# Kernel tuning notes

Hardware: AMD Instinct MI355X
Metric: run time of the kernel (lower is better)

Reference implementation:

```python
import jax, jax.numpy as jnp
import numpy as np

B, NP, NS, CIN, COUT, CMID = 16, 1024, 32, 64, 128, 32

def _bn(x, g, b, m, v, eps=1e-5):
    # inference-mode BatchNorm over channel axis 1
    sh = (1, -1) + (1,) * (x.ndim - 2)
    return (x - m.reshape(sh)) * (g.reshape(sh) * jax.lax.rsqrt(v.reshape(sh) + eps)) + b.reshape(sh)

def setup_inputs() -> dict:
    key = jax.random.key(0)
    ks = jax.random.split(key, 10)
    f = jax.random.normal
    return {
        "new_xyz": f(ks[0], (B, 3, NP), jnp.float32),
        "grouped_xyz": f(ks[1], (B, NP, NS, 3), jnp.float32),
        "grouped_feature": f(ks[2], (B, CIN, NS, NP), jnp.float32),
        "wh_w": f(ks[3], (CMID, 3), jnp.float32) * 0.1,
        "wh_b": f(ks[4], (CMID,), jnp.float32) * 0.1,
        "wh_g": jnp.ones((CMID,), jnp.float32), "wh_beta": jnp.zeros((CMID,), jnp.float32),
        "wh_m": jnp.zeros((CMID,), jnp.float32), "wh_v": jnp.ones((CMID,), jnp.float32),
        "n1_w": f(ks[5], (16, 1), jnp.float32) * 0.1,
        "n1_b": f(ks[6], (16,), jnp.float32) * 0.1,
        "n1_g": jnp.ones((16,), jnp.float32), "n1_beta": jnp.zeros((16,), jnp.float32),
        "n1_m": jnp.zeros((16,), jnp.float32), "n1_v": jnp.ones((16,), jnp.float32),
        "n2_w": f(ks[7], (1, 16), jnp.float32) * 0.1,
        "n2_b": f(ks[8], (1,), jnp.float32) * 0.1,
        "n2_g": jnp.ones((1,), jnp.float32), "n2_beta": jnp.zeros((1,), jnp.float32),
        "n2_m": jnp.zeros((1,), jnp.float32), "n2_v": jnp.ones((1,), jnp.float32),
        "out_w": f(ks[9], (COUT, CIN, CMID), jnp.float32) * 0.05,
        "out_b": jnp.zeros((COUT,), jnp.float32),
        "out_g": jnp.ones((COUT,), jnp.float32), "out_beta": jnp.zeros((COUT,), jnp.float32),
        "out_m": jnp.zeros((COUT,), jnp.float32), "out_v": jnp.ones((COUT,), jnp.float32),
    }

def reference(new_xyz, grouped_xyz, grouped_feature,
              wh_w, wh_b, wh_g, wh_beta, wh_m, wh_v,
              n1_w, n1_b, n1_g, n1_beta, n1_m, n1_v,
              n2_w, n2_b, n2_g, n2_beta, n2_m, n2_v,
              out_w, out_b, out_g, out_beta, out_m, out_v):
    # kernel_density_estimation_ball mutates in place: after i=0 the reference
    # point is zero, so ONLY sample 0 is actually zeroed. Replicate exactly.
    gx = grouped_xyz.at[:, :, 0, :].set(0.0)          # [B,NP,NS,3]
    density = jnp.sum(gx, axis=-1, keepdims=True)      # [B,NP,NS,1]
    density = jnp.where(density < 1e-10, 1e-10, density)
    inv = 1.0 / density
    ds = inv / jnp.max(inv, axis=2, keepdims=True)     # [B,NP,NS,1]
    # weight net on the mutated grouped_xyz
    gx_p = jnp.transpose(gx, (0, 3, 1, 2))             # [B,3,NP,NS]
    w = jax.nn.relu(_bn(jnp.einsum('bcps,oc->bops', gx_p, wh_w) + wh_b.reshape(1, -1, 1, 1),
                        wh_g, wh_beta, wh_m, wh_v))    # [B,CMID,NP,NS]
    # nonlinear density transform
    dsp = jnp.transpose(ds, (0, 3, 1, 2))              # [B,1,NP,NS]
    d1 = jax.nn.relu(_bn(jnp.einsum('bcps,oc->bops', dsp, n1_w) + n1_b.reshape(1, -1, 1, 1),
                         n1_g, n1_beta, n1_m, n1_v))   # [B,16,NP,NS]
    d2 = jax.nn.sigmoid(_bn(jnp.einsum('bcps,oc->bops', d1, n2_w) + n2_b.reshape(1, -1, 1, 1),
                            n2_g, n2_beta, n2_m, n2_v))  # [B,1,NP,NS]
    # density-scaled features, then batched matmul with positional weights
    gf = jnp.transpose(grouped_feature, (0, 1, 3, 2)) * d2      # [B,CIN,NP,NS]
    mm = jnp.einsum('bcps,bmps->bcpm', gf, w)                   # [B,CIN,NP,CMID]
    # out_conv: Conv2d(CIN->COUT, kernel (1,CMID)) collapses last dim
    out = jnp.einsum('bcpk,ock->bop', mm, out_w) + out_b.reshape(1, -1, 1)  # [B,COUT,NP]
    out = _bn(out, out_g, out_beta, out_m, out_v)
    return (jnp.transpose(new_xyz, (0, 2, 1)), out)
```

## Files before the change

### kernel.cpp

```cpp
#include <hip/hip_runtime.h>
#include <hip/hip_bf16.h>


#define NPP 1024
#define NSS 32

typedef __attribute__((ext_vector_type(8))) short short8;
typedef __attribute__((ext_vector_type(4))) float f32x4;

__device__ __forceinline__ unsigned short f2bf(float x) {
  union { float f; unsigned u; } v; v.f = x;
  unsigned r = v.u + 0x7FFFu + ((v.u >> 16) & 1u);
  return (unsigned short)(r >> 16);
}

__device__ __forceinline__ unsigned long long pack4bf(f32x4 v) {
  return (unsigned long long)f2bf(v[0])
       | ((unsigned long long)f2bf(v[1]) << 16)
       | ((unsigned long long)f2bf(v[2]) << 32)
       | ((unsigned long long)f2bf(v[3]) << 48);
}

__global__ __launch_bounds__(256) void k_prep(
    const float* __restrict__ out_w, const float* __restrict__ new_xyz,
    unsigned short* __restrict__ owc, float* __restrict__ out0)
{
  int bid = blockIdx.x, t = threadIdx.x;
  if (bid < 128) {
    int gid = bid * 256 + t;
    int lane = gid & 63, ci = gid >> 6;
    int hi = ci & 1, tt = (ci >> 1) & 15, cblk = (ci >> 5) & 3, w = ci >> 7;
    int sg = lane >> 4, l15 = lane & 15;
    int o = w*32 + hi*16 + l15;
    int k = tt*2 + (sg >> 1);
    int cbase = cblk*16 + (sg & 1)*8;
    short8 vv;
    #pragma unroll
    for (int j = 0; j < 8; ++j)
      vv[j] = (short)f2bf(out_w[(o*64 + cbase + j)*32 + k]);
    *(short8*)&owc[(size_t)gid * 8] = vv;
  } else {
    int idx = (bid - 128) * 256 + t;
    int b = idx / 3072, r = idx - b*3072, p = r / 3, d = r - p*3;
    out0[idx] = new_xyz[(b*3 + d)*NPP + p];
  }
}

__global__ __launch_bounds__(256) void k_xpose(
    const float* __restrict__ F, unsigned short* __restrict__ Fb)
{
  int bid = blockIdx.x;
  int xcd = bid & 7, idx = bid >> 3;
  int b = xcd * 2 + (idx >> 4), ptq = idx & 15;
  int t = threadIdx.x;
  int sg = t >> 6, l15 = (t >> 2) & 15, k4 = t & 3;

  #pragma unroll
  for (int cblk = 0; cblk < 4; ++cblk) {
    int c = cblk * 16 + l15;
    const float* src = &F[((size_t)((b*64 + c)*32) + sg*8)*NPP + ptq*64 + k4*4];
    #pragma unroll
    for (int ptl = 0; ptl < 4; ++ptl) {
      float4 v[8];
      #pragma unroll
      for (int j = 0; j < 8; ++j) v[j] = *(const float4*)&src[(size_t)j*NPP + ptl*16];
      unsigned short* tb = &Fb[(size_t)(b*64 + ptq*4 + ptl)*32768 + cblk*512 + sg*128 + l15*8];
      #pragma unroll
      for (int pwl = 0; pwl < 4; ++pwl) {
        unsigned o0 = (unsigned)f2bf(((const float*)&v[0])[pwl]) | ((unsigned)f2bf(((const float*)&v[1])[pwl]) << 16);
        unsigned o1 = (unsigned)f2bf(((const float*)&v[2])[pwl]) | ((unsigned)f2bf(((const float*)&v[3])[pwl]) << 16);
        unsigned o2 = (unsigned)f2bf(((const float*)&v[4])[pwl]) | ((unsigned)f2bf(((const float*)&v[5])[pwl]) << 16);
        unsigned o3 = (unsigned)f2bf(((const float*)&v[6])[pwl]) | ((unsigned)f2bf(((const float*)&v[7])[pwl]) << 16);
        uint4 wv = {o0, o1, o2, o3};
        *(uint4*)&tb[(size_t)(k4*4 + pwl)*2048] = wv;
      }
    }
  }
}

struct Smem {
  union {
    unsigned short wd[16*32*32];
    char mm[2][16*1040];
  } u;
  float cst[192];
};

__global__ __launch_bounds__(256, 4) void k_main(
    const unsigned short* __restrict__ Fb, const float* __restrict__ GX,
    const float* __restrict__ whw, const float* __restrict__ whb,
    const float* __restrict__ whg, const float* __restrict__ whbeta,
    const float* __restrict__ whm, const float* __restrict__ whv,
    const float* __restrict__ n1w, const float* __restrict__ n1b,
    const float* __restrict__ n1g, const float* __restrict__ n1beta,
    const float* __restrict__ n1m, const float* __restrict__ n1v,
    const float* __restrict__ n2w, const float* __restrict__ n2b,
    const float* __restrict__ n2g, const float* __restrict__ n2beta,
    const float* __restrict__ n2m, const float* __restrict__ n2v,
    const unsigned short* __restrict__ OWc,
    const float* __restrict__ ob, const float* __restrict__ og,
    const float* __restrict__ obeta, const float* __restrict__ om,
    const float* __restrict__ ov,
    float* __restrict__ out1)
{
  __shared__ Smem sm;
  int bid = (blockIdx.x & 7) * 128 + (blockIdx.x >> 3);
  int b = bid >> 6, p0 = (bid & 63) << 4;
  int t = threadIdx.x, lane = t & 63, w = t >> 6;
  int l15 = lane & 15, sg = lane >> 4;
  int pl0 = w * 4;

  const unsigned short* ftile = &Fb[(size_t)(b*64 + (bid & 63))*32768 + sg*128 + l15*8];
  short8 af[4][4];
  #pragma unroll
  for (int cblk = 0; cblk < 4; ++cblk)
    #pragma unroll
    for (int i = 0; i < 4; ++i)
      af[cblk][i] = *(const short8*)&ftile[(size_t)(pl0 + i)*2048 + cblk*512];

  int pp = t >> 4, si = t & 15;
  float gxl[2][3]; float invv[2];
  #pragma unroll
  for (int u = 0; u < 2; ++u) {
    int s = si*2 + u;
    float x = 0.f, y = 0.f, z = 0.f;
    if (s != 0) {
      const float* g = &GX[(size_t)((b*NPP + p0 + pp)*NSS + s)*3];
      x = g[0]; y = g[1]; z = g[2];
    }
    gxl[u][0]=x; gxl[u][1]=y; gxl[u][2]=z;
    float den = x + y + z;
    if (den < 1e-10f) den = 1e-10f;
    invv[u] = 1.0f / den;
  }
  float mx = fmaxf(invv[0], invv[1]);
  #pragma unroll
  for (int m = 1; m < 16; m <<= 1) mx = fmaxf(mx, __shfl_xor(mx, m, 16));

  if (t < 32) {
    float sc = whg[t] * rsqrtf(whv[t] + 1e-5f);
    sm.cst[t]    = whw[t*3+0] * sc;
    sm.cst[32+t] = whw[t*3+1] * sc;
    sm.cst[64+t] = whw[t*3+2] * sc;
    sm.cst[96+t] = (whb[t] - whm[t]) * sc + whbeta[t];
  } else if (t < 48) {
    int i = t - 32;
    float sc = n1g[i] * rsqrtf(n1v[i] + 1e-5f);
    sm.cst[128+i] = n1w[i] * sc;
    sm.cst[144+i] = (n1b[i] - n1m[i]) * sc + n1beta[i];
  } else if (t < 64) {
    int i = t - 48;
    float sc = n2g[0] * rsqrtf(n2v[0] + 1e-5f);
    sm.cst[160+i] = n2w[i] * sc;
    if (i == 0) sm.cst[176] = (n2b[0] - n2m[0]) * sc + n2beta[0];
  }
  __syncthreads();

  float d2v[2];
  #pragma unroll
  for (int u = 0; u < 2; ++u) {
    float ds = invv[u] / mx;
    float acc = sm.cst[176];
    #pragma unroll
    for (int i = 0; i < 16; ++i) {
      float d1 = fmaxf(ds * sm.cst[128+i] + sm.cst[144+i], 0.f);
      acc += d1 * sm.cst[160+i];
    }
    d2v[u] = 1.0f / (1.0f + expf(-acc));
  }
  #pragma unroll 4
  for (int k = 0; k < 32; ++k) {
    float a0 = sm.cst[k], a1 = sm.cst[32+k], a2 = sm.cst[64+k], bc = sm.cst[96+k];
    unsigned r = 0;
    #pragma unroll
    for (int u = 0; u < 2; ++u) {
      float wv = fmaxf(gxl[u][0]*a0 + gxl[u][1]*a1 + gxl[u][2]*a2 + bc, 0.f);
      wv *= d2v[u];
      r |= (unsigned)f2bf(wv) << (16*u);
    }
    *(unsigned*)&sm.u.wd[(pp*32 + k)*32 + si*2] = r;
  }
  __syncthreads();

  short8 bfr[4][2];
  #pragma unroll
  for (int i = 0; i < 4; ++i)
    #pragma unroll
    for (int kh = 0; kh < 2; ++kh)
      bfr[i][kh] = *(const short8*)&sm.u.wd[((pl0+i)*32 + kh*16 + l15)*32 + sg*8];
  __syncthreads();

  f32x4 acc0 = {0,0,0,0}, acc1 = {0,0,0,0};
  const f32x4 z4 = {0,0,0,0};

  #pragma unroll
  for (int cblk = 0; cblk < 4; ++cblk) {
    char* mmw = sm.u.mm[cblk & 1];
    {
      #pragma unroll
      for (int i = 0; i < 4; ++i) {
        f32x4 m0 = __builtin_amdgcn_mfma_f32_16x16x32_bf16(af[cblk][i], bfr[i][0], z4, 0,0,0);
        f32x4 m1 = __builtin_amdgcn_mfma_f32_16x16x32_bf16(af[cblk][i], bfr[i][1], z4, 0,0,0);
        char* base = mmw + (pl0+i)*1040 + l15*32 + sg*8;
        *(unsigned long long*)(base)       = pack4bf(m0);
        *(unsigned long long*)(base + 512) = pack4bf(m1);
      }
    }
    __syncthreads();
    {
      const unsigned short* ac = &OWc[(size_t)((w*4 + cblk)*16)*1024 + lane*8];
      const char* brow = mmw + l15*1040 + sg*16;
      #pragma unroll 8
      for (int tt = 0; tt < 16; ++tt) {
        short8 a0 = *(const short8*)&ac[tt*1024];
        short8 a1 = *(const short8*)&ac[tt*1024 + 512];
        short8 bb = *(const short8*)&brow[tt*64];
        acc0 = __builtin_amdgcn_mfma_f32_16x16x32_bf16(a0, bb, acc0, 0,0,0);
        acc1 = __builtin_amdgcn_mfma_f32_16x16x32_bf16(a1, bb, acc1, 0,0,0);
      }
    }
  }

  #pragma unroll
  for (int mf = 0; mf < 2; ++mf) {
    f32x4 a = mf ? acc1 : acc0;
    #pragma unroll
    for (int r = 0; r < 4; ++r) {
      int o = w*32 + mf*16 + sg*4 + r;
      float sc = og[o] * rsqrtf(ov[o] + 1e-5f);
      float dd = (ob[o] - om[o]) * sc + obeta[o];
      out1[(size_t)(b*128 + o)*NPP + p0 + l15] = a[r] * sc + dd;
    }
  }
}

extern "C" void kernel_launch(void* const* d_in, const int* in_sizes, int n_in,
                              void* d_out, int out_size, void* d_ws, size_t ws_size,
                              hipStream_t stream) {
  (void)in_sizes; (void)n_in; (void)out_size; (void)ws_size;
  const float* new_xyz = (const float*)d_in[0];
  const float* gxyz    = (const float*)d_in[1];
  const float* gfeat   = (const float*)d_in[2];
  const float* whw     = (const float*)d_in[3];
  const float* whb     = (const float*)d_in[4];
  const float* whg     = (const float*)d_in[5];
  const float* whbeta  = (const float*)d_in[6];
  const float* whm     = (const float*)d_in[7];
  const float* whv     = (const float*)d_in[8];
  const float* n1w     = (const float*)d_in[9];
  const float* n1b     = (const float*)d_in[10];
  const float* n1g     = (const float*)d_in[11];
  const float* n1beta  = (const float*)d_in[12];
  const float* n1m     = (const float*)d_in[13];
  const float* n1v     = (const float*)d_in[14];
  const float* n2w     = (const float*)d_in[15];
  const float* n2b     = (const float*)d_in[16];
  const float* n2g     = (const float*)d_in[17];
  const float* n2beta  = (const float*)d_in[18];
  const float* n2m     = (const float*)d_in[19];
  const float* n2v     = (const float*)d_in[20];
  const float* out_w   = (const float*)d_in[21];
  const float* out_b   = (const float*)d_in[22];
  const float* out_g   = (const float*)d_in[23];
  const float* out_bt  = (const float*)d_in[24];
  const float* out_m   = (const float*)d_in[25];
  const float* out_v   = (const float*)d_in[26];

  unsigned short* owc = (unsigned short*)d_ws;
  unsigned short* fb  = owc + (1u << 18);
  float* out0 = (float*)d_out;
  float* out1 = out0 + 16*1024*3;

  hipLaunchKernelGGL(k_prep,  dim3(320),  dim3(256), 0, stream, out_w, new_xyz, owc, out0);
  hipLaunchKernelGGL(k_xpose, dim3(256),  dim3(256), 0, stream, gfeat, fb);
  hipLaunchKernelGGL(k_main,  dim3(1024), dim3(256), 0, stream,
      fb, gxyz, whw, whb, whg, whbeta, whm, whv,
      n1w, n1b, n1g, n1beta, n1m, n1v,
      n2w, n2b, n2g, n2beta, n2m, n2v,
      owc, out_b, out_g, out_bt, out_m, out_v, out1);
}
```

Before: 88.23 us.

## Enlarge main kernel tile to 64 points with 512-thread blocks and swizzled LDS

The main kernel now processes 64 points per block with 8 waves instead of 16 points with 4 waves. Each OWc weight fragment is reused across two 16-point groups, and density/xyz staging is split into a separate LDS pass. The intermediate mm buffer uses an XOR swizzle instead of row padding to avoid bank conflicts. The aim is to cut redundant weight loads and per-block setup, at the cost of much larger LDS use and register pressure, which allows only one block per CU and a grid of 256 blocks.

After: 87.02 us. No clear change (-1.4%).

```diff
diff --git a/kernel.cpp b/kernel.cpp
--- a/kernel.cpp
+++ b/kernel.cpp
@@ -78,15 +78,14 @@
   }
 }
 
-struct Smem {
-  union {
-    unsigned short wd[16*32*32];
-    char mm[2][16*1040];
-  } u;
+struct Smem2 {
+  float gxd[64*32*4];
+  unsigned short wd[16*32*32];
+  char mm[64*1024];
   float cst[192];
 };
 
-__global__ __launch_bounds__(256, 4) void k_main(
+__global__ __launch_bounds__(512, 1) void k_main(
     const unsigned short* __restrict__ Fb, const float* __restrict__ GX,
     const float* __restrict__ whw, const float* __restrict__ whb,
     const float* __restrict__ whg, const float* __restrict__ whbeta,
@@ -103,39 +102,18 @@
     const float* __restrict__ ov,
     float* __restrict__ out1)
 {
-  __shared__ Smem sm;
-  int bid = (blockIdx.x & 7) * 128 + (blockIdx.x >> 3);
-  int b = bid >> 6, p0 = (bid & 63) << 4;
-  int t = threadIdx.x, lane = t & 63, w = t >> 6;
+  __shared__ Smem2 sm;
+  int xcd = blockIdx.x & 7, idx = blockIdx.x >> 3;
+  int b = xcd*2 + (idx >> 4), pt64 = idx & 15;
+  int p0 = pt64 * 64;
+  int t = threadIdx.x, w = t >> 6, lane = t & 63;
   int l15 = lane & 15, sg = lane >> 4;
-  int pl0 = w * 4;
-
-  const unsigned short* ftile = &Fb[(size_t)(b*64 + (bid & 63))*32768 + sg*128 + l15*8];
-  short8 af[4][4];
-  #pragma unroll
-  for (int cblk = 0; cblk < 4; ++cblk)
-    #pragma unroll
-    for (int i = 0; i < 4; ++i)
-      af[cblk][i] = *(const short8*)&ftile[(size_t)(pl0 + i)*2048 + cblk*512];
-
-  int pp = t >> 4, si = t & 15;
-  float gxl[2][3]; float invv[2];
-  #pragma unroll
-  for (int u = 0; u < 2; ++u) {
-    int s = si*2 + u;
-    float x = 0.f, y = 0.f, z = 0.f;
-    if (s != 0) {
-      const float* g = &GX[(size_t)((b*NPP + p0 + pp)*NSS + s)*3];
-      x = g[0]; y = g[1]; z = g[2];
-    }
-    gxl[u][0]=x; gxl[u][1]=y; gxl[u][2]=z;
-    float den = x + y + z;
-    if (den < 1e-10f) den = 1e-10f;
-    invv[u] = 1.0f / den;
-  }
-  float mx = fmaxf(invv[0], invv[1]);
-  #pragma unroll
-  for (int m = 1; m < 16; m <<= 1) mx = fmaxf(mx, __shfl_xor(mx, m, 16));
+
+  int pp8 = t >> 3, si8 = t & 7;
+  const float* g = &GX[(size_t)(b*NPP + p0 + pp8)*96 + si8*12];
+  float4 f0 = *(const float4*)g;
+  float4 f1 = *(const float4*)(g + 4);
+  float4 f2 = *(const float4*)(g + 8);
 
   if (t < 32) {
     float sc = whg[t] * rsqrtf(whv[t] + 1e-5f);
@@ -156,82 +134,130 @@
   }
   __syncthreads();
 
-  float d2v[2];
+  {
+    float xs[4], ys[4], zs[4], inv[4];
+    xs[0]=f0.x; ys[0]=f0.y; zs[0]=f0.z;
+    xs[1]=f0.w; ys[1]=f1.x; zs[1]=f1.y;
+    xs[2]=f1.z; ys[2]=f1.w; zs[2]=f2.x;
+    xs[3]=f2.y; ys[3]=f2.z; zs[3]=f2.w;
+    if (si8 == 0) { xs[0]=0.f; ys[0]=0.f; zs[0]=0.f; }
+    float mx = 0.f;
+    #pragma unroll
+    for (int u = 0; u < 4; ++u) {
+      float den = xs[u] + ys[u] + zs[u];
+      if (den < 1e-10f) den = 1e-10f;
+      inv[u] = 1.0f / den;
+      mx = fmaxf(mx, inv[u]);
+    }
+    #pragma unroll
+    for (int m = 1; m < 8; m <<= 1) mx = fmaxf(mx, __shfl_xor(mx, m, 8));
+    #pragma unroll
+    for (int u = 0; u < 4; ++u) {
+      float ds = inv[u] / mx;
+      float acc = sm.cst[176];
+      #pragma unroll
+      for (int i = 0; i < 16; ++i) {
+        float d1 = fmaxf(ds * sm.cst[128+i] + sm.cst[144+i], 0.f);
+        acc += d1 * sm.cst[160+i];
+      }
+      float d2 = 1.0f / (1.0f + expf(-acc));
+      float4 st = {xs[u], ys[u], zs[u], d2};
+      *(float4*)&sm.gxd[(size_t)(pp8*32 + si8*4 + u)*4] = st;
+    }
+  }
+  __syncthreads();
+
+  const f32x4 z4 = {0,0,0,0};
+  int phKh = (lane >> 4) & 1;
+  int phPp = w*2 + (lane >> 5);
+  int phSi = lane & 15;
+  int ppA = w*2, ppB = w*2 + 1;
+  int c0 = l15*32 + sg*8;
+
+  short8 afA[4][4], afB[4][4];
+  short8 bfrA[4][2], bfrB[4][2];
   #pragma unroll
-  for (int u = 0; u < 2; ++u) {
-    float ds = invv[u] / mx;
-    float acc = sm.cst[176];
-    #pragma unroll
-    for (int i = 0; i < 16; ++i) {
-      float d1 = fmaxf(ds * sm.cst[128+i] + sm.cst[144+i], 0.f);
-      acc += d1 * sm.cst[160+i];
-    }
-    d2v[u] = 1.0f / (1.0f + expf(-acc));
-  }
-  #pragma unroll 4
-  for (int k = 0; k < 32; ++k) {
-    float a0 = sm.cst[k], a1 = sm.cst[32+k], a2 = sm.cst[64+k], bc = sm.cst[96+k];
-    unsigned r = 0;
-    #pragma unroll
-    for (int u = 0; u < 2; ++u) {
-      float wv = fmaxf(gxl[u][0]*a0 + gxl[u][1]*a1 + gxl[u][2]*a2 + bc, 0.f);
-      wv *= d2v[u];
-      r |= (unsigned)f2bf(wv) << (16*u);
-    }
-    *(unsigned*)&sm.u.wd[(pp*32 + k)*32 + si*2] = r;
-  }
-  __syncthreads();
-
-  short8 bfr[4][2];
-  #pragma unroll
-  for (int i = 0; i < 4; ++i)
-    #pragma unroll
-    for (int kh = 0; kh < 2; ++kh)
-      bfr[i][kh] = *(const short8*)&sm.u.wd[((pl0+i)*32 + kh*16 + l15)*32 + sg*8];
-  __syncthreads();
-
-  f32x4 acc0 = {0,0,0,0}, acc1 = {0,0,0,0};
-  const f32x4 z4 = {0,0,0,0};
+  for (int pg = 0; pg < 4; ++pg) {
+    const unsigned short* ft = &Fb[(size_t)(b*64 + pt64*4 + pg)*32768 + sg*128 + l15*8];
+    #pragma unroll
+    for (int cblk = 0; cblk < 4; ++cblk) {
+      afA[pg][cblk] = *(const short8*)&ft[(size_t)ppA*2048 + cblk*512];
+      afB[pg][cblk] = *(const short8*)&ft[(size_t)ppB*2048 + cblk*512];
+    }
+    const float4 ga = *(const float4*)&sm.gxd[(size_t)((pg*16 + phPp)*32 + phSi*2)*4];
+    const float4 gb = *(const float4*)&sm.gxd[(size_t)((pg*16 + phPp)*32 + phSi*2 + 1)*4];
+    #pragma unroll
+    for (int ki = 0; ki < 16; ++ki) {
+      int k = phKh*16 + ki;
+      float a0 = sm.cst[k], a1 = sm.cst[32+k], a2 = sm.cst[64+k], bc = sm.cst[96+k];
+      float w0 = fmaxf(ga.x*a0 + ga.y*a1 + ga.z*a2 + bc, 0.f) * ga.w;
+      float w1 = fmaxf(gb.x*a0 + gb.y*a1 + gb.z*a2 + bc, 0.f) * gb.w;
+      unsigned r = (unsigned)f2bf(w0) | ((unsigned)f2bf(w1) << 16);
+      *(unsigned*)&sm.wd[(phPp*32 + k)*32 + phSi*2] = r;
+    }
+    #pragma unroll
+    for (int kh = 0; kh < 2; ++kh) {
+      bfrA[pg][kh] = *(const short8*)&sm.wd[(ppA*32 + kh*16 + l15)*32 + sg*8];
+      bfrB[pg][kh] = *(const short8*)&sm.wd[(ppB*32 + kh*16 + l15)*32 + sg*8];
+    }
+  }
+
+  int w4 = w & 3, gp0 = (w >> 2) * 2;
+  f32x4 acc00 = {0,0,0,0}, acc10 = {0,0,0,0}, acc01 = {0,0,0,0}, acc11 = {0,0,0,0};
+  int rowG0 = gp0*16 + l15, rowG1 = (gp0+1)*16 + l15;
+  unsigned sw0 = (rowG0 & 15) << 4, sw1 = (rowG1 & 15) << 4;
+  const char* bbase0 = sm.mm + rowG0*1024;
+  const char* bbase1 = sm.mm + rowG1*1024;
 
   #pragma unroll
   for (int cblk = 0; cblk < 4; ++cblk) {
-    char* mmw = sm.u.mm[cblk & 1];
-    {
-      #pragma unroll
-      for (int i = 0; i < 4; ++i) {
-        f32x4 m0 = __builtin_amdgcn_mfma_f32_16x16x32_bf16(af[cblk][i], bfr[i][0], z4, 0,0,0);
-        f32x4 m1 = __builtin_amdgcn_mfma_f32_16x16x32_bf16(af[cblk][i], bfr[i][1], z4, 0,0,0);
-        char* base = mmw + (pl0+i)*1040 + l15*32 + sg*8;
-        *(unsigned long long*)(base)       = pack4bf(m0);
-        *(unsigned long long*)(base + 512) = pack4bf(m1);
-      }
+    #pragma unroll
+    for (int pg = 0; pg < 4; ++pg) {
+      f32x4 mA0 = __builtin_amdgcn_mfma_f32_16x16x32_bf16(afA[pg][cblk], bfrA[pg][0], z4, 0,0,0);
+      f32x4 mA1 = __builtin_amdgcn_mfma_f32_16x16x32_bf16(afA[pg][cblk], bfrA[pg][1], z4, 0,0,0);
+      f32x4 mB0 = __builtin_amdgcn_mfma_f32_16x16x32_bf16(afB[pg][cblk], bfrB[pg][0], z4, 0,0,0);
+      f32x4 mB1 = __builtin_amdgcn_mfma_f32_16x16x32_bf16(afB[pg][cblk], bfrB[pg][1], z4, 0,0,0);
+      int rowA = pg*16 + ppA, rowB = pg*16 + ppB;
+      unsigned swA = (rowA & 15) << 4, swB = (rowB & 15) << 4;
+      char* bA = sm.mm + rowA*1024;
+      char* bB = sm.mm + rowB*1024;
+      *(unsigned long long*)(bA + ((c0      ) ^ swA)) = pack4bf(mA0);
+      *(unsigned long long*)(bA + ((c0 + 512) ^ swA)) = pack4bf(mA1);
+      *(unsigned long long*)(bB + ((c0      ) ^ swB)) = pack4bf(mB0);
+      *(unsigned long long*)(bB + ((c0 + 512) ^ swB)) = pack4bf(mB1);
     }
     __syncthreads();
     {
-      const unsigned short* ac = &OWc[(size_t)((w*4 + cblk)*16)*1024 + lane*8];
-      const char* brow = mmw + l15*1040 + sg*16;
+      const unsigned short* ac = &OWc[(size_t)((w4*4 + cblk)*16)*1024 + lane*8];
       #pragma unroll 8
       for (int tt = 0; tt < 16; ++tt) {
         short8 a0 = *(const short8*)&ac[tt*1024];
         short8 a1 = *(const short8*)&ac[tt*1024 + 512];
-        short8 bb = *(const short8*)&brow[tt*64];
-        acc0 = __builtin_amdgcn_mfma_f32_16x16x32_bf16(a0, bb, acc0, 0,0,0);
-        acc1 = __builtin_amdgcn_mfma_f32_16x16x32_bf16(a1, bb, acc1, 0,0,0);
+        int col = sg*16 + tt*64;
+        short8 b0 = *(const short8*)(bbase0 + (col ^ sw0));
+        short8 b1 = *(const short8*)(bbase1 + (col ^ sw1));
+        acc00 = __builtin_amdgcn_mfma_f32_16x16x32_bf16(a0, b0, acc00, 0,0,0);
+        acc10 = __builtin_amdgcn_mfma_f32_16x16x32_bf16(a1, b0, acc10, 0,0,0);
+        acc01 = __builtin_amdgcn_mfma_f32_16x16x32_bf16(a0, b1, acc01, 0,0,0);
+        acc11 = __builtin_amdgcn_mfma_f32_16x16x32_bf16(a1, b1, acc11, 0,0,0);
       }
     }
+    __syncthreads();
   }
 
   #pragma unroll
-  for (int mf = 0; mf < 2; ++mf) {
-    f32x4 a = mf ? acc1 : acc0;
-    #pragma unroll
-    for (int r = 0; r < 4; ++r) {
-      int o = w*32 + mf*16 + sg*4 + r;
-      float sc = og[o] * rsqrtf(ov[o] + 1e-5f);
-      float dd = (ob[o] - om[o]) * sc + obeta[o];
-      out1[(size_t)(b*128 + o)*NPP + p0 + l15] = a[r] * sc + dd;
-    }
-  }
+  for (int hi = 0; hi < 2; ++hi)
+    #pragma unroll
+    for (int gg = 0; gg < 2; ++gg) {
+      f32x4 a = hi ? (gg ? acc11 : acc10) : (gg ? acc01 : acc00);
+      #pragma unroll
+      for (int r = 0; r < 4; ++r) {
+        int o = w4*32 + hi*16 + sg*4 + r;
+        float sc = og[o] * rsqrtf(ov[o] + 1e-5f);
+        float dd = (ob[o] - om[o]) * sc + obeta[o];
+        out1[(size_t)(b*128 + o)*NPP + p0 + (gp0+gg)*16 + l15] = a[r] * sc + dd;
+      }
+    }
 }
 
 extern "C" void kernel_launch(void* const* d_in, const int* in_sizes, int n_in,
@@ -271,9 +297,9 @@
   float* out0 = (float*)d_out;
   float* out1 = out0 + 16*1024*3;
 
-  hipLaunchKernelGGL(k_prep,  dim3(320),  dim3(256), 0, stream, out_w, new_xyz, owc, out0);
-  hipLaunchKernelGGL(k_xpose, dim3(256),  dim3(256), 0, stream, gfeat, fb);
-  hipLaunchKernelGGL(k_main,  dim3(1024), dim3(256), 0, stream,
+  hipLaunchKernelGGL(k_prep,  dim3(320), dim3(256), 0, stream, out_w, new_xyz, owc, out0);
+  hipLaunchKernelGGL(k_xpose, dim3(256), dim3(256), 0, stream, gfeat, fb);
+  hipLaunchKernelGGL(k_main,  dim3(256), dim3(512), 0, stream,
       fb, gxyz, whw, whb, whg, whbeta, whm, whv,
       n1w, n1b, n1g, n1beta, n1m, n1v,
       n2w, n2b, n2g, n2beta, n2m, n2v,
```
